# Kernel optimization log

Hardware: AMD Instinct MI355X
Metric: run time of the kernel (lower is better)

The kernel has to match this reference:

```python
import jax, jax.numpy as jnp
import numpy as np

B, N, IN_DIM = 2, 512, 512
MEM, HID = 300, 64
NEG_SLOPE = 0.01


def setup_inputs() -> dict:
    key = jax.random.key(0)
    ks = jax.random.split(key, 10)
    feature = jax.random.normal(ks[0], (B, N, IN_DIM), dtype=jnp.float32)
    adj = jax.random.randint(ks[1], (B, N, N), 0, 2).astype(jnp.float32)
    s = 0.05
    # per-layer node projections W[l]
    w0 = jax.random.normal(ks[2], (IN_DIM, MEM), dtype=jnp.float32) * s
    b0 = jnp.zeros((MEM,), dtype=jnp.float32)
    w1 = jax.random.normal(ks[3], (MEM, MEM), dtype=jnp.float32) * s
    b1 = jnp.zeros((MEM,), dtype=jnp.float32)
    # shared attention MLP (afcs): Linear(2*MEM, HID) -> ReLU -> Linear(HID, 1)
    a1_w = jax.random.normal(ks[4], (2 * MEM, HID), dtype=jnp.float32) * s
    a1_b = jnp.zeros((HID,), dtype=jnp.float32)
    a2_w = jax.random.normal(ks[5], (HID, 1), dtype=jnp.float32) * s
    a2_b = jnp.zeros((1,), dtype=jnp.float32)
    return {"feature": feature, "adj": adj, "w0": w0, "b0": b0, "w1": w1,
            "b1": b1, "a1_w": a1_w, "a1_b": a1_b, "a2_w": a2_w, "a2_b": a2_b}


def _gat_layer(h_in, adj, w, b, a1_w, a1_b, a2_w, a2_b):
    h = h_in @ w + b                                   # (B,N,M)
    # cat([h_i, h_j]) @ a1_w split into the two halves (same math, no N^2*2M tensor)
    s_i = h @ a1_w[:MEM]                               # (B,N,H)
    s_j = h @ a1_w[MEM:]                               # (B,N,H)
    z = jax.nn.relu(s_i[:, :, None, :] + s_j[:, None, :, :] + a1_b)   # (B,N,N,H)
    e = (z @ a2_w)[..., 0] + a2_b[0]                   # (B,N,N)
    e = jax.nn.leaky_relu(e, negative_slope=NEG_SLOPE)
    b_, n_ = adj.shape[0], adj.shape[1]
    dmask = adj.reshape(b_, n_ * n_)
    logits = e.reshape(b_, n_ * n_) * dmask + (1.0 - dmask) * (-1e30)
    # NOTE: softmax over ALL N*N flattened edges (faithful to original dim=1)
    att = jax.nn.softmax(logits, axis=1).reshape(b_, n_, n_)
    return jnp.einsum('bij,bjd->bid', att, h)


def reference(feature, adj, w0, b0, w1, b1, a1_w, a1_b, a2_w, a2_b):
    f = _gat_layer(feature, adj, w0, b0, a1_w, a1_b, a2_w, a2_b)
    f = _gat_layer(f, adj, w1, b1, a1_w, a1_b, a2_w, a2_b)  # dropout = identity (eval)
    return f
```

## Files before the change

kernel.cpp:

```cpp
#include <hip/hip_runtime.h>

namespace {

constexpr int B_  = 2;
constexpr int N_  = 512;
constexpr int IN_ = 512;
constexpr int M_  = 300;
constexpr int H_  = 64;
constexpr float SLOPE_ = 0.01f;

constexpr long OFF_W0AI = 0;
constexpr long OFF_W0AJ = OFF_W0AI + 512L * 64;
constexpr long OFF_W1AI = OFF_W0AJ + 512L * 64;
constexpr long OFF_W1AJ = OFF_W1AI + 300L * 64;
constexpr long OFF_BSI0 = OFF_W1AJ + 300L * 64;
constexpr long OFF_BSJ0 = OFF_BSI0 + 64;
constexpr long OFF_BSI1 = OFF_BSJ0 + 64;
constexpr long OFF_BSJ1 = OFF_BSI1 + 64;
constexpr long OFF_H0   = OFF_BSJ1 + 64;
constexpr long OFF_SI0  = OFF_H0   + 1024L * 300;
constexpr long OFF_SJ0  = OFF_SI0  + 1024L * 64;
constexpr long OFF_F1   = OFF_SJ0  + 1024L * 64;
constexpr long OFF_H1   = OFF_F1   + 1024L * 300;
constexpr long OFF_SI1  = OFF_H1   + 1024L * 300;
constexpr long OFF_SJ1  = OFF_SI1  + 1024L * 64;
constexpr long OFF_ZP0  = OFF_SJ1  + 1024L * 64;
constexpr long OFF_ZP1  = OFF_ZP0  + 512;
constexpr long OFF_P0   = OFF_ZP1  + 512;
constexpr long OFF_P1   = OFF_P0   + 2L * 512 * 512;

struct Jobs {
    const float* A[8]; const float* W[8]; const float* bias[8]; const float* Zp[8];
    float* C[8];
    int K[8]; int lda[8]; int Cc[8]; int R[8];
    int off[8]; int njobs;
};

__global__ __launch_bounds__(256)
void gemm_multi(Jobs jb)
{
    __shared__ __align__(16) float As[16][68];
    __shared__ __align__(16) float Ws[16][64];

    const int bid = blockIdx.x;
    int j = jb.njobs - 1;
    while (j > 0 && bid < jb.off[j]) --j;
    const int local = bid - jb.off[j];

    const float* __restrict__ A = jb.A[j];
    const float* __restrict__ W = jb.W[j];
    const float* bias = jb.bias[j];
    const float* Zp   = jb.Zp[j];
    float* __restrict__ C = jb.C[j];
    const int K = jb.K[j], lda = jb.lda[j], Cc = jb.Cc[j], R = jb.R[j];

    const int tx   = (Cc + 63) >> 6;
    const int row0 = (local / tx) * 64;
    const int col0 = (local % tx) * 64;

    const int t    = threadIdx.x;
    const int arow = min(row0 + (t >> 2), R - 1);
    const int akg  = (t & 3) * 4;
    const int wk   = t >> 4;
    const int wc   = (t & 15) * 4;
    const int tm0  = (t >> 4) * 4;
    const int tn0  = (t & 15) * 4;

    auto loadA = [&](int k0) -> float4 {
        const int k = k0 + akg;
        if (k + 3 < K) return *(const float4*)(A + (long)arow * lda + k);
        float tv[4];
        #pragma unroll
        for (int v = 0; v < 4; ++v)
            tv[v] = (k + v < K) ? A[(long)arow * lda + k + v] : 0.0f;
        return make_float4(tv[0], tv[1], tv[2], tv[3]);
    };
    auto loadW = [&](int k0) -> float4 {
        const int gk = k0 + wk;
        const int c  = col0 + wc;
        if (gk < K && c + 3 < Cc) return *(const float4*)(W + (long)gk * Cc + c);
        float tv[4];
        #pragma unroll
        for (int v = 0; v < 4; ++v)
            tv[v] = (gk < K && c + v < Cc) ? W[(long)gk * Cc + c + v] : 0.0f;
        return make_float4(tv[0], tv[1], tv[2], tv[3]);
    };

    float acc[4][4] = {};
    float4 av = loadA(0);
    float4 wv = loadW(0);

    for (int k0 = 0; k0 < K; k0 += 16) {
        As[akg + 0][t >> 2] = av.x;
        As[akg + 1][t >> 2] = av.y;
        As[akg + 2][t >> 2] = av.z;
        As[akg + 3][t >> 2] = av.w;
        *(float4*)&Ws[wk][wc] = wv;
        __syncthreads();

        if (k0 + 16 < K) {
            av = loadA(k0 + 16);
            wv = loadW(k0 + 16);
        }

        #pragma unroll
        for (int k = 0; k < 16; ++k) {
            const float4 a4 = *(const float4*)&As[k][tm0];
            const float4 w4 = *(const float4*)&Ws[k][tn0];
            const float aa[4] = {a4.x, a4.y, a4.z, a4.w};
            const float ww[4] = {w4.x, w4.y, w4.z, w4.w};
            #pragma unroll
            for (int i = 0; i < 4; ++i)
                #pragma unroll
                for (int jj = 0; jj < 4; ++jj)
                    acc[i][jj] = fmaf(aa[i], ww[jj], acc[i][jj]);
        }
        __syncthreads();
    }

    float scale = 1.0f;
    if (Zp != nullptr) {
        float s0 = 0.f, s1 = 0.f, s2 = 0.f, s3 = 0.f;
        for (int u = 0; u < 256; u += 4) {
            s0 += Zp[u]; s1 += Zp[u + 1]; s2 += Zp[u + 2]; s3 += Zp[u + 3];
        }
        scale = 1.0f / ((s0 + s1) + (s2 + s3));
    }
    const int cbase = col0 + tn0;
    float bv[4] = {0.f, 0.f, 0.f, 0.f};
    if (bias != nullptr) {
        #pragma unroll
        for (int u = 0; u < 4; ++u)
            if (cbase + u < Cc) bv[u] = bias[cbase + u];
    }
    #pragma unroll
    for (int i = 0; i < 4; ++i) {
        const int r = row0 + tm0 + i;
        if (r < R) {
            if (cbase + 3 < Cc) {
                float4 o;
                o.x = fmaf(acc[i][0], scale, bv[0]);
                o.y = fmaf(acc[i][1], scale, bv[1]);
                o.z = fmaf(acc[i][2], scale, bv[2]);
                o.w = fmaf(acc[i][3], scale, bv[3]);
                *(float4*)(C + (long)r * Cc + cbase) = o;
            } else {
                #pragma unroll
                for (int u = 0; u < 4; ++u)
                    if (cbase + u < Cc)
                        C[(long)r * Cc + cbase + u] = fmaf(acc[i][u], scale, bv[u]);
            }
        }
    }
}

__global__ __launch_bounds__(256)
void attn_p_kernel(const float* __restrict__ si, const float* __restrict__ sj,
                   const float* __restrict__ adj, const float* __restrict__ a2w,
                   const float* __restrict__ a2b, float* __restrict__ p,
                   float* __restrict__ Zpart)
{
    __shared__ __align__(16) float Si[32][68];
    __shared__ __align__(16) float Sj[32][68];

    const int b  = blockIdx.z;
    const int i0 = blockIdx.y * 32;
    const int j0 = blockIdx.x * 32;
    const int t  = threadIdx.x;

    {
        const int r  = t >> 3;
        const int hc = (t & 7) * 8;
        const float* gi = si + ((long)(b * N_ + i0 + r)) * H_ + hc;
        const float* gj = sj + ((long)(b * N_ + j0 + r)) * H_ + hc;
        *(float4*)&Si[r][hc]     = *(const float4*)(gi);
        *(float4*)&Si[r][hc + 4] = *(const float4*)(gi + 4);
        *(float4*)&Sj[r][hc]     = *(const float4*)(gj);
        *(float4*)&Sj[r][hc + 4] = *(const float4*)(gj + 4);
    }
    __syncthreads();

    const int i  = t >> 3;
    const int jl = t & 7;

    float e[4] = {0.f, 0.f, 0.f, 0.f};
    #pragma unroll
    for (int h0 = 0; h0 < H_; h0 += 4) {
        const float4 a4 = *(const float4*)&Si[i][h0];
        const float w0v = a2w[h0 + 0];
        const float w1v = a2w[h0 + 1];
        const float w2v = a2w[h0 + 2];
        const float w3v = a2w[h0 + 3];
        #pragma unroll
        for (int u = 0; u < 4; ++u) {
            const float4 b4 = *(const float4*)&Sj[jl + 8 * u][h0];
            e[u] = fmaf(fmaxf(a4.x + b4.x, 0.f), w0v, e[u]);
            e[u] = fmaf(fmaxf(a4.y + b4.y, 0.f), w1v, e[u]);
            e[u] = fmaf(fmaxf(a4.z + b4.z, 0.f), w2v, e[u]);
            e[u] = fmaf(fmaxf(a4.w + b4.w, 0.f), w3v, e[u]);
        }
    }

    const float a2bv = a2b[0];
    const long rowbase = ((long)(b * N_ + i0 + i)) * N_ + j0 + jl;
    float lsum = 0.f;
    #pragma unroll
    for (int u = 0; u < 4; ++u) {
        float ev = e[u] + a2bv;
        ev = (ev >= 0.f) ? ev : SLOPE_ * ev;
        const float m  = adj[rowbase + 8 * u];
        const float pv = m * __expf(ev);
        p[rowbase + 8 * u] = pv;
        lsum += pv;
    }

    #pragma unroll
    for (int off = 32; off > 0; off >>= 1)
        lsum += __shfl_down(lsum, off, 64);
    __shared__ float red[4];
    if ((t & 63) == 0) red[t >> 6] = lsum;
    __syncthreads();
    if (t == 0)
        Zpart[b * 256 + blockIdx.y * 16 + blockIdx.x] =
            red[0] + red[1] + red[2] + red[3];
}

}

extern "C" void kernel_launch(void* const* d_in, const int* in_sizes, int n_in,
                              void* d_out, int out_size, void* d_ws, size_t ws_size,
                              hipStream_t stream)
{
    const float* feature = (const float*)d_in[0];
    const float* adj     = (const float*)d_in[1];
    const float* w0      = (const float*)d_in[2];
    const float* b0      = (const float*)d_in[3];
    const float* w1      = (const float*)d_in[4];
    const float* b1      = (const float*)d_in[5];
    const float* a1w     = (const float*)d_in[6];
    const float* a1b     = (const float*)d_in[7];
    const float* a2w     = (const float*)d_in[8];
    const float* a2b     = (const float*)d_in[9];
    float* out = (float*)d_out;
    float* ws  = (float*)d_ws;

    float* cW0Ai = ws + OFF_W0AI;
    float* cW0Aj = ws + OFF_W0AJ;
    float* cW1Ai = ws + OFF_W1AI;
    float* cW1Aj = ws + OFF_W1AJ;
    float* bsi0  = ws + OFF_BSI0;
    float* bsj0  = ws + OFF_BSJ0;
    float* bsi1  = ws + OFF_BSI1;
    float* bsj1  = ws + OFF_BSJ1;
    float* h0    = ws + OFF_H0;
    float* si0   = ws + OFF_SI0;
    float* sj0   = ws + OFF_SJ0;
    float* f1    = ws + OFF_F1;
    float* h1    = ws + OFF_H1;
    float* si1   = ws + OFF_SI1;
    float* sj1   = ws + OFF_SJ1;
    float* Zp0   = ws + OFF_ZP0;
    float* Zp1   = ws + OFF_ZP1;
    float* p0    = ws + OFF_P0;
    float* p1    = ws + OFF_P1;

    const float* Ai = a1w;
    const float* Aj = a1w + (long)M_ * H_;

    auto set_job = [](Jobs& jb, int j, const float* A, const float* W,
                      const float* bias, const float* Zp, float* C,
                      int K, int lda, int Cc, int R, int& tiles) {
        jb.A[j] = A; jb.W[j] = W; jb.bias[j] = bias; jb.Zp[j] = Zp; jb.C[j] = C;
        jb.K[j] = K; jb.lda[j] = lda; jb.Cc[j] = Cc; jb.R[j] = R;
        jb.off[j] = tiles;
        tiles += ((R + 63) / 64) * ((Cc + 63) / 64);
    };

    {
        Jobs jb; int tiles = 0;
        set_job(jb, 0, w0, Ai, nullptr, nullptr, cW0Ai, M_, M_, H_, IN_, tiles);
        set_job(jb, 1, w0, Aj, nullptr, nullptr, cW0Aj, M_, M_, H_, IN_, tiles);
        set_job(jb, 2, w1, Ai, nullptr, nullptr, cW1Ai, M_, M_, H_, M_,  tiles);
        set_job(jb, 3, w1, Aj, nullptr, nullptr, cW1Aj, M_, M_, H_, M_,  tiles);
        set_job(jb, 4, b0, Ai, nullptr, nullptr, bsi0,  M_, M_, H_, 1,   tiles);
        set_job(jb, 5, b0, Aj, a1b,     nullptr, bsj0,  M_, M_, H_, 1,   tiles);
        set_job(jb, 6, b1, Ai, nullptr, nullptr, bsi1,  M_, M_, H_, 1,   tiles);
        set_job(jb, 7, b1, Aj, a1b,     nullptr, bsj1,  M_, M_, H_, 1,   tiles);
        jb.njobs = 8;
        gemm_multi<<<dim3(tiles), dim3(256), 0, stream>>>(jb);
    }

    {
        Jobs jb; int tiles = 0;
        set_job(jb, 0, feature, w0,    b0,   nullptr, h0,  IN_, IN_, M_, 1024, tiles);
        set_job(jb, 1, feature, cW0Ai, bsi0, nullptr, si0, IN_, IN_, H_, 1024, tiles);
        set_job(jb, 2, feature, cW0Aj, bsj0, nullptr, sj0, IN_, IN_, H_, 1024, tiles);
        jb.njobs = 3;
        gemm_multi<<<dim3(tiles), dim3(256), 0, stream>>>(jb);
    }

    attn_p_kernel<<<dim3(16, 16, B_), dim3(256), 0, stream>>>(
        si0, sj0, adj, a2w, a2b, p0, Zp0);

    {
        Jobs jb; int tiles = 0;
        set_job(jb, 0, p0,               h0,              nullptr, Zp0,       f1,
                N_, N_, M_, N_, tiles);
        set_job(jb, 1, p0 + (long)N_*N_, h0 + (long)N_*M_, nullptr, Zp0 + 256,
                f1 + (long)N_*M_, N_, N_, M_, N_, tiles);
        jb.njobs = 2;
        gemm_multi<<<dim3(tiles), dim3(256), 0, stream>>>(jb);
    }

    {
        Jobs jb; int tiles = 0;
        set_job(jb, 0, f1, w1,    b1,   nullptr, h1,  M_, M_, M_, 1024, tiles);
        set_job(jb, 1, f1, cW1Ai, bsi1, nullptr, si1, M_, M_, H_, 1024, tiles);
        set_job(jb, 2, f1, cW1Aj, bsj1, nullptr, sj1, M_, M_, H_, 1024, tiles);
        jb.njobs = 3;
        gemm_multi<<<dim3(tiles), dim3(256), 0, stream>>>(jb);
    }

    attn_p_kernel<<<dim3(16, 16, B_), dim3(256), 0, stream>>>(
        si1, sj1, adj, a2w, a2b, p1, Zp1);

    {
        Jobs jb; int tiles = 0;
        set_job(jb, 0, p1,               h1,              nullptr, Zp1,       out,
                N_, N_, M_, N_, tiles);
        set_job(jb, 1, p1 + (long)N_*N_, h1 + (long)N_*M_, nullptr, Zp1 + 256,
                out + (long)N_*M_, N_, N_, M_, N_, tiles);
        jb.njobs = 2;
        gemm_multi<<<dim3(tiles), dim3(256), 0, stream>>>(jb);
    }
}
```

Measured before the change: 197.7 us.

## Split-K GEMMs into partial halves, fuse attention into mega kernel, reassociate layer-2 score projections

Replaces separate GEMM and attention kernels with a single multi-job mega kernel that can run GEMM tiles and attention-score tiles in the same launch. Each GEMM is split along K into two halves written to separate buffers, which consumers sum on load, so more blocks are available. Layer-2 score projections are reassociated as p·(h0·W1A) so they can run alongside the layer-1 aggregation. The final aggregation uses a smaller 32-row tile GEMM for more blocks. The aim is fewer serial launches and better GPU fill, at the cost of extra partial-buffer traffic, doubled loads and more complex job dispatch.

```diff
diff --git a/kernel.cpp b/kernel.cpp
--- a/kernel.cpp
+++ b/kernel.cpp
@@ -2,227 +2,400 @@
 
 namespace {
 
-constexpr int B_  = 2;
-constexpr int N_  = 512;
-constexpr int IN_ = 512;
-constexpr int M_  = 300;
-constexpr int H_  = 64;
+constexpr int N_ = 512;
+constexpr int M_ = 300;
+constexpr int H_ = 64;
 constexpr float SLOPE_ = 0.01f;
-
-constexpr long OFF_W0AI = 0;
-constexpr long OFF_W0AJ = OFF_W0AI + 512L * 64;
-constexpr long OFF_W1AI = OFF_W0AJ + 512L * 64;
-constexpr long OFF_W1AJ = OFF_W1AI + 300L * 64;
-constexpr long OFF_BSI0 = OFF_W1AJ + 300L * 64;
-constexpr long OFF_BSJ0 = OFF_BSI0 + 64;
-constexpr long OFF_BSI1 = OFF_BSJ0 + 64;
-constexpr long OFF_BSJ1 = OFF_BSI1 + 64;
-constexpr long OFF_H0   = OFF_BSJ1 + 64;
-constexpr long OFF_SI0  = OFF_H0   + 1024L * 300;
-constexpr long OFF_SJ0  = OFF_SI0  + 1024L * 64;
-constexpr long OFF_F1   = OFF_SJ0  + 1024L * 64;
-constexpr long OFF_H1   = OFF_F1   + 1024L * 300;
-constexpr long OFF_SI1  = OFF_H1   + 1024L * 300;
-constexpr long OFF_SJ1  = OFF_SI1  + 1024L * 64;
-constexpr long OFF_ZP0  = OFF_SJ1  + 1024L * 64;
-constexpr long OFF_ZP1  = OFF_ZP0  + 512;
-constexpr long OFF_P0   = OFF_ZP1  + 512;
-constexpr long OFF_P1   = OFF_P0   + 2L * 512 * 512;
-
+constexpr long NN = 262144;
+constexpr long NM = 153600;
+constexpr long NH = 32768;
+
+constexpr long O_CW0AI_A = 0;
+constexpr long O_CW0AI_B = O_CW0AI_A + 512L*64;
+constexpr long O_CW0AJ_A = O_CW0AI_B + 512L*64;
+constexpr long O_CW0AJ_B = O_CW0AJ_A + 512L*64;
+constexpr long O_CW1AI_A = O_CW0AJ_B + 512L*64;
+constexpr long O_CW1AI_B = O_CW1AI_A + 300L*64;
+constexpr long O_CW1AJ_A = O_CW1AI_B + 300L*64;
+constexpr long O_CW1AJ_B = O_CW1AJ_A + 300L*64;
+constexpr long O_BS      = O_CW1AJ_B + 300L*64;
+constexpr long O_H0_A  = O_BS + 8*64;
+constexpr long O_H0_B  = O_H0_A + 1024L*300;
+constexpr long O_SI0_A = O_H0_B + 1024L*300;
+constexpr long O_SI0_B = O_SI0_A + 1024L*64;
+constexpr long O_SJ0_A = O_SI0_B + 1024L*64;
+constexpr long O_SJ0_B = O_SJ0_A + 1024L*64;
+constexpr long O_GI_A  = O_SJ0_B + 1024L*64;
+constexpr long O_GI_B  = O_GI_A + 1024L*64;
+constexpr long O_GJ_A  = O_GI_B + 1024L*64;
+constexpr long O_GJ_B  = O_GJ_A + 1024L*64;
+constexpr long O_F1_A  = O_GJ_B + 1024L*64;
+constexpr long O_F1_B  = O_F1_A + 1024L*300;
+constexpr long O_H1_A  = O_F1_B + 1024L*300;
+constexpr long O_H1_B  = O_H1_A + 1024L*300;
+constexpr long O_SI1_A = O_H1_B + 1024L*300;
+constexpr long O_SI1_B = O_SI1_A + 1024L*64;
+constexpr long O_SJ1_A = O_SI1_B + 1024L*64;
+constexpr long O_SJ1_B = O_SJ1_A + 1024L*64;
+constexpr long O_ZP0   = O_SJ1_B + 1024L*64;
+constexpr long O_ZP1   = O_ZP0 + 512;
+constexpr long O_P0    = O_ZP1 + 512;
+constexpr long O_P1    = O_P0 + 2L*NN;
+
+constexpr int MAXJ = 12;
 struct Jobs {
-    const float* A[8]; const float* W[8]; const float* bias[8]; const float* Zp[8];
-    float* C[8];
-    int K[8]; int lda[8]; int Cc[8]; int R[8];
-    int off[8]; int njobs;
+    const float* A[MAXJ]; const float* A2[MAXJ];
+    const float* W[MAXJ]; const float* W2[MAXJ];
+    const float* bias[MAXJ]; const float* bias2[MAXJ];
+    const float* Zp[MAXJ];
+    float* C[MAXJ]; float* Zout[MAXJ];
+    int ks[MAXJ], ke[MAXJ], lda[MAXJ], Cc[MAXJ], R[MAXJ], off[MAXJ], type[MAXJ];
+    int njobs;
 };
 
+__device__ __forceinline__ float job_scale(const float* Zp)
+{
+    if (Zp == nullptr) return 1.0f;
+    float s0 = 0.f, s1 = 0.f, s2 = 0.f, s3 = 0.f;
+    for (int u = 0; u < 256; u += 4) {
+        s0 += Zp[u]; s1 += Zp[u + 1]; s2 += Zp[u + 2]; s3 += Zp[u + 3];
+    }
+    return 1.0f / ((s0 + s1) + (s2 + s3));
+}
+
 __global__ __launch_bounds__(256)
-void gemm_multi(Jobs jb)
+void mega(Jobs jb, const float* __restrict__ a2w, const float* __restrict__ a2b)
 {
-    __shared__ __align__(16) float As[16][68];
-    __shared__ __align__(16) float Ws[16][64];
+    __shared__ __align__(16) char sm[17424];
 
     const int bid = blockIdx.x;
     int j = jb.njobs - 1;
     while (j > 0 && bid < jb.off[j]) --j;
     const int local = bid - jb.off[j];
-
-    const float* __restrict__ A = jb.A[j];
-    const float* __restrict__ W = jb.W[j];
-    const float* bias = jb.bias[j];
-    const float* Zp   = jb.Zp[j];
+    const int t = threadIdx.x;
+
+    if (jb.type[j] == 0) {
+        float (*As)[68] = reinterpret_cast<float(*)[68]>(sm);
+        float (*Ws)[64] = reinterpret_cast<float(*)[64]>(sm + 16*68*4);
+
+        const float* __restrict__ A  = jb.A[j];
+        const float* __restrict__ A2 = jb.A2[j];
+        const float* __restrict__ W  = jb.W[j];
+        const float* __restrict__ W2 = jb.W2[j];
+        float* __restrict__ C = jb.C[j];
+        const int ks = jb.ks[j], ke = jb.ke[j];
+        const int lda = jb.lda[j], Cc = jb.Cc[j], R = jb.R[j];
+
+        const int tx   = (Cc + 63) >> 6;
+        const int row0 = (local / tx) * 64;
+        const int col0 = (local % tx) * 64;
+
+        const int arow = min(row0 + (t >> 2), R - 1);
+        const int akg  = (t & 3) * 4;
+        const int wk   = t >> 4;
+        const int wc   = (t & 15) * 4;
+        const int tm0  = (t >> 4) * 4;
+        const int tn0  = (t & 15) * 4;
+
+        auto loadA1 = [&](const float* P, int k0) -> float4 {
+            const int k = k0 + akg;
+            if (k + 3 < ke) return *(const float4*)(P + (long)arow * lda + k);
+            float tv[4];
+            #pragma unroll
+            for (int v = 0; v < 4; ++v)
+                tv[v] = (k + v < ke) ? P[(long)arow * lda + k + v] : 0.0f;
+            return make_float4(tv[0], tv[1], tv[2], tv[3]);
+        };
+        auto loadW1 = [&](const float* P, int k0) -> float4 {
+            const int gk = k0 + wk;
+            const int c  = col0 + wc;
+            if (gk < ke && c + 3 < Cc) return *(const float4*)(P + (long)gk * Cc + c);
+            float tv[4];
+            #pragma unroll
+            for (int v = 0; v < 4; ++v)
+                tv[v] = (gk < ke && c + v < Cc) ? P[(long)gk * Cc + c + v] : 0.0f;
+            return make_float4(tv[0], tv[1], tv[2], tv[3]);
+        };
+        auto loadA = [&](int k0) -> float4 {
+            float4 r = loadA1(A, k0);
+            if (A2) {
+                const float4 r2 = loadA1(A2, k0);
+                r.x += r2.x; r.y += r2.y; r.z += r2.z; r.w += r2.w;
+            }
+            return r;
+        };
+        auto loadW = [&](int k0) -> float4 {
+            float4 r = loadW1(W, k0);
+            if (W2) {
+                const float4 r2 = loadW1(W2, k0);
+                r.x += r2.x; r.y += r2.y; r.z += r2.z; r.w += r2.w;
+            }
+            return r;
+        };
+
+        float acc[4][4] = {};
+        float4 av = loadA(ks);
+        float4 wv = loadW(ks);
+
+        for (int k0 = ks; k0 < ke; k0 += 16) {
+            As[akg + 0][t >> 2] = av.x;
+            As[akg + 1][t >> 2] = av.y;
+            As[akg + 2][t >> 2] = av.z;
+            As[akg + 3][t >> 2] = av.w;
+            *(float4*)&Ws[wk][wc] = wv;
+            __syncthreads();
+
+            if (k0 + 16 < ke) {
+                av = loadA(k0 + 16);
+                wv = loadW(k0 + 16);
+            }
+
+            #pragma unroll
+            for (int k = 0; k < 16; ++k) {
+                const float4 a4 = *(const float4*)&As[k][tm0];
+                const float4 w4 = *(const float4*)&Ws[k][tn0];
+                const float aa[4] = {a4.x, a4.y, a4.z, a4.w};
+                const float ww[4] = {w4.x, w4.y, w4.z, w4.w};
+                #pragma unroll
+                for (int i = 0; i < 4; ++i)
+                    #pragma unroll
+                    for (int q = 0; q < 4; ++q)
+                        acc[i][q] = fmaf(aa[i], ww[q], acc[i][q]);
+            }
+            __syncthreads();
+        }
+
+        const float scale = job_scale(jb.Zp[j]);
+        const int cbase = col0 + tn0;
+        float bv[4] = {0.f, 0.f, 0.f, 0.f};
+        if (jb.bias[j] != nullptr && ks == 0) {
+            const float* b1p = jb.bias[j];
+            const float* b2p = jb.bias2[j];
+            #pragma unroll
+            for (int u = 0; u < 4; ++u)
+                if (cbase + u < Cc)
+                    bv[u] = b1p[cbase + u] + (b2p ? b2p[cbase + u] : 0.0f);
+        }
+        #pragma unroll
+        for (int i = 0; i < 4; ++i) {
+            const int r = row0 + tm0 + i;
+            if (r < R) {
+                if (cbase + 3 < Cc) {
+                    float4 o;
+                    o.x = fmaf(acc[i][0], scale, bv[0]);
+                    o.y = fmaf(acc[i][1], scale, bv[1]);
+                    o.z = fmaf(acc[i][2], scale, bv[2]);
+                    o.w = fmaf(acc[i][3], scale, bv[3]);
+                    *(float4*)(C + (long)r * Cc + cbase) = o;
+                } else {
+                    #pragma unroll
+                    for (int u = 0; u < 4; ++u)
+                        if (cbase + u < Cc)
+                            C[(long)r * Cc + cbase + u] = fmaf(acc[i][u], scale, bv[u]);
+                }
+            }
+        }
+    } else {
+        float (*Si)[68] = reinterpret_cast<float(*)[68]>(sm);
+        float (*Sj)[68] = reinterpret_cast<float(*)[68]>(sm + 32*68*4);
+        float* red = reinterpret_cast<float*>(sm + 2*32*68*4);
+
+        const int b  = local >> 8;
+        const int r8 = local & 255;
+        const int i0 = (r8 >> 4) * 32;
+        const int j0 = (r8 & 15) * 32;
+
+        const float* siA = jb.A[j]  + (long)b * NH;
+        const float* siB = jb.A2[j] + (long)b * NH;
+        const float* sjA = jb.W[j]  + (long)b * NH;
+        const float* sjB = jb.W2[j] + (long)b * NH;
+        const float* adjb = jb.bias[j] + (long)b * NN;
+        float* pb = jb.C[j] + (long)b * NN;
+
+        {
+            const int r  = t >> 3;
+            const int hc = (t & 7) * 8;
+            const long oi = (long)(i0 + r) * H_ + hc;
+            const long oj = (long)(j0 + r) * H_ + hc;
+            #pragma unroll
+            for (int h = 0; h < 2; ++h) {
+                float4 v1 = *(const float4*)(siA + oi + 4*h);
+                const float4 v2 = *(const float4*)(siB + oi + 4*h);
+                v1.x += v2.x; v1.y += v2.y; v1.z += v2.z; v1.w += v2.w;
+                *(float4*)&Si[r][hc + 4*h] = v1;
+                float4 u1 = *(const float4*)(sjA + oj + 4*h);
+                const float4 u2 = *(const float4*)(sjB + oj + 4*h);
+                u1.x += u2.x; u1.y += u2.y; u1.z += u2.z; u1.w += u2.w;
+                *(float4*)&Sj[r][hc + 4*h] = u1;
+            }
+        }
+        __syncthreads();
+
+        const int i  = t >> 3;
+        const int jl = t & 7;
+
+        float e[4] = {0.f, 0.f, 0.f, 0.f};
+        #pragma unroll
+        for (int h0 = 0; h0 < H_; h0 += 4) {
+            const float4 a4 = *(const float4*)&Si[i][h0];
+            const float w0v = a2w[h0 + 0];
+            const float w1v = a2w[h0 + 1];
+            const float w2v = a2w[h0 + 2];
+            const float w3v = a2w[h0 + 3];
+            #pragma unroll
+            for (int u = 0; u < 4; ++u) {
+                const float4 b4 = *(const float4*)&Sj[jl + 8 * u][h0];
+                e[u] = fmaf(fmaxf(a4.x + b4.x, 0.f), w0v, e[u]);
+                e[u] = fmaf(fmaxf(a4.y + b4.y, 0.f), w1v, e[u]);
+                e[u] = fmaf(fmaxf(a4.z + b4.z, 0.f), w2v, e[u]);
+                e[u] = fmaf(fmaxf(a4.w + b4.w, 0.f), w3v, e[u]);
+            }
+        }
+
+        const float a2bv = a2b[0];
+        const long rowbase = (long)(i0 + i) * N_ + j0 + jl;
+        float lsum = 0.f;
+        #pragma unroll
+        for (int u = 0; u < 4; ++u) {
+            float ev = e[u] + a2bv;
+            ev = (ev >= 0.f) ? ev : SLOPE_ * ev;
+            const float m  = adjb[rowbase + 8 * u];
+            const float pv = m * __expf(ev);
+            pb[rowbase + 8 * u] = pv;
+            lsum += pv;
+        }
+
+        #pragma unroll
+        for (int off = 32; off > 0; off >>= 1)
+            lsum += __shfl_down(lsum, off, 64);
+        if ((t & 63) == 0) red[t >> 6] = lsum;
+        __syncthreads();
+        if (t == 0)
+            jb.Zout[j][b * 256 + r8] = red[0] + red[1] + red[2] + red[3];
+    }
+}
+
+__global__ __launch_bounds__(256)
+void gemm32(Jobs jb)
+{
+    __shared__ __align__(16) float As[32][38];
+    __shared__ __align__(16) float Ws[32][64];
+
+    const int bid = blockIdx.x;
+    int j = jb.njobs - 1;
+    while (j > 0 && bid < jb.off[j]) --j;
+    const int local = bid - jb.off[j];
+
+    const float* __restrict__ A  = jb.A[j];
+    const float* __restrict__ W  = jb.W[j];
+    const float* __restrict__ W2 = jb.W2[j];
     float* __restrict__ C = jb.C[j];
-    const int K = jb.K[j], lda = jb.lda[j], Cc = jb.Cc[j], R = jb.R[j];
+    const int ke = jb.ke[j], lda = jb.lda[j], Cc = jb.Cc[j], R = jb.R[j];
 
     const int tx   = (Cc + 63) >> 6;
-    const int row0 = (local / tx) * 64;
+    const int row0 = (local / tx) * 32;
     const int col0 = (local % tx) * 64;
 
     const int t    = threadIdx.x;
-    const int arow = min(row0 + (t >> 2), R - 1);
-    const int akg  = (t & 3) * 4;
+    const int sr   = t >> 3;
+    const int sk   = (t & 7) * 4;
+    const int arow = min(row0 + sr, R - 1);
     const int wk   = t >> 4;
     const int wc   = (t & 15) * 4;
-    const int tm0  = (t >> 4) * 4;
+    const int tm0  = (t >> 4) * 2;
     const int tn0  = (t & 15) * 4;
 
     auto loadA = [&](int k0) -> float4 {
-        const int k = k0 + akg;
-        if (k + 3 < K) return *(const float4*)(A + (long)arow * lda + k);
+        const int k = k0 + sk;
+        if (k + 3 < ke) return *(const float4*)(A + (long)arow * lda + k);
         float tv[4];
         #pragma unroll
         for (int v = 0; v < 4; ++v)
-            tv[v] = (k + v < K) ? A[(long)arow * lda + k + v] : 0.0f;
+            tv[v] = (k + v < ke) ? A[(long)arow * lda + k + v] : 0.0f;
         return make_float4(tv[0], tv[1], tv[2], tv[3]);
     };
-    auto loadW = [&](int k0) -> float4 {
-        const int gk = k0 + wk;
+    auto loadW = [&](int k0, int s) -> float4 {
+        const int gk = k0 + wk + 16 * s;
         const int c  = col0 + wc;
-        if (gk < K && c + 3 < Cc) return *(const float4*)(W + (long)gk * Cc + c);
-        float tv[4];
+        float4 r = make_float4(0.f, 0.f, 0.f, 0.f);
+        if (gk < ke) {
+            if (c + 3 < Cc) {
+                r = *(const float4*)(W + (long)gk * Cc + c);
+                if (W2) {
+                    const float4 r2 = *(const float4*)(W2 + (long)gk * Cc + c);
+                    r.x += r2.x; r.y += r2.y; r.z += r2.z; r.w += r2.w;
+                }
+            } else {
+                float tv[4];
+                #pragma unroll
+                for (int v = 0; v < 4; ++v) {
+                    tv[v] = (c + v < Cc) ? W[(long)gk * Cc + c + v] : 0.0f;
+                    if (W2 && c + v < Cc) tv[v] += W2[(long)gk * Cc + c + v];
+                }
+                r = make_float4(tv[0], tv[1], tv[2], tv[3]);
+            }
+        }
+        return r;
+    };
+
+    float acc[2][4] = {};
+    float4 av  = loadA(0);
+    float4 wv0 = loadW(0, 0);
+    float4 wv1 = loadW(0, 1);
+
+    for (int k0 = 0; k0 < ke; k0 += 32) {
+        As[sk + 0][sr] = av.x;
+        As[sk + 1][sr] = av.y;
+        As[sk + 2][sr] = av.z;
+        As[sk + 3][sr] = av.w;
+        *(float4*)&Ws[wk][wc]      = wv0;
+        *(float4*)&Ws[wk + 16][wc] = wv1;
+        __syncthreads();
+
+        if (k0 + 32 < ke) {
+            av  = loadA(k0 + 32);
+            wv0 = loadW(k0 + 32, 0);
+            wv1 = loadW(k0 + 32, 1);
+        }
+
         #pragma unroll
-        for (int v = 0; v < 4; ++v)
-            tv[v] = (gk < K && c + v < Cc) ? W[(long)gk * Cc + c + v] : 0.0f;
-        return make_float4(tv[0], tv[1], tv[2], tv[3]);
-    };
-
-    float acc[4][4] = {};
-    float4 av = loadA(0);
-    float4 wv = loadW(0);
-
-    for (int k0 = 0; k0 < K; k0 += 16) {
-        As[akg + 0][t >> 2] = av.x;
-        As[akg + 1][t >> 2] = av.y;
-        As[akg + 2][t >> 2] = av.z;
-        As[akg + 3][t >> 2] = av.w;
-        *(float4*)&Ws[wk][wc] = wv;
+        for (int k = 0; k < 32; ++k) {
+            const float a0 = As[k][tm0];
+            const float a1 = As[k][tm0 + 1];
+            const float4 w4 = *(const float4*)&Ws[k][tn0];
+            acc[0][0] = fmaf(a0, w4.x, acc[0][0]);
+            acc[0][1] = fmaf(a0, w4.y, acc[0][1]);
+            acc[0][2] = fmaf(a0, w4.z, acc[0][2]);
+            acc[0][3] = fmaf(a0, w4.w, acc[0][3]);
+            acc[1][0] = fmaf(a1, w4.x, acc[1][0]);
+            acc[1][1] = fmaf(a1, w4.y, acc[1][1]);
+            acc[1][2] = fmaf(a1, w4.z, acc[1][2]);
+            acc[1][3] = fmaf(a1, w4.w, acc[1][3]);
+        }
         __syncthreads();
-
-        if (k0 + 16 < K) {
-            av = loadA(k0 + 16);
-            wv = loadW(k0 + 16);
-        }
-
-        #pragma unroll
-        for (int k = 0; k < 16; ++k) {
-            const float4 a4 = *(const float4*)&As[k][tm0];
-            const float4 w4 = *(const float4*)&Ws[k][tn0];
-            const float aa[4] = {a4.x, a4.y, a4.z, a4.w};
-            const float ww[4] = {w4.x, w4.y, w4.z, w4.w};
-            #pragma unroll
-            for (int i = 0; i < 4; ++i)
-                #pragma unroll
-                for (int jj = 0; jj < 4; ++jj)
-                    acc[i][jj] = fmaf(aa[i], ww[jj], acc[i][jj]);
-        }
-        __syncthreads();
-    }
-
-    float scale = 1.0f;
-    if (Zp != nullptr) {
-        float s0 = 0.f, s1 = 0.f, s2 = 0.f, s3 = 0.f;
-        for (int u = 0; u < 256; u += 4) {
-            s0 += Zp[u]; s1 += Zp[u + 1]; s2 += Zp[u + 2]; s3 += Zp[u + 3];
-        }
-        scale = 1.0f / ((s0 + s1) + (s2 + s3));
-    }
+    }
+
+    const float scale = job_scale(jb.Zp[j]);
     const int cbase = col0 + tn0;
-    float bv[4] = {0.f, 0.f, 0.f, 0.f};
-    if (bias != nullptr) {
-        #pragma unroll
-        for (int u = 0; u < 4; ++u)
-            if (cbase + u < Cc) bv[u] = bias[cbase + u];
-    }
     #pragma unroll
-    for (int i = 0; i < 4; ++i) {
+    for (int i = 0; i < 2; ++i) {
         const int r = row0 + tm0 + i;
         if (r < R) {
             if (cbase + 3 < Cc) {
                 float4 o;
-                o.x = fmaf(acc[i][0], scale, bv[0]);
-                o.y = fmaf(acc[i][1], scale, bv[1]);
-                o.z = fmaf(acc[i][2], scale, bv[2]);
-                o.w = fmaf(acc[i][3], scale, bv[3]);
+                o.x = acc[i][0] * scale;
+                o.y = acc[i][1] * scale;
+                o.z = acc[i][2] * scale;
+                o.w = acc[i][3] * scale;
                 *(float4*)(C + (long)r * Cc + cbase) = o;
             } else {
                 #pragma unroll
                 for (int u = 0; u < 4; ++u)
                     if (cbase + u < Cc)
-                        C[(long)r * Cc + cbase + u] = fmaf(acc[i][u], scale, bv[u]);
-            }
-        }
-    }
-}
-
-__global__ __launch_bounds__(256)
-void attn_p_kernel(const float* __restrict__ si, const float* __restrict__ sj,
-                   const float* __restrict__ adj, const float* __restrict__ a2w,
-                   const float* __restrict__ a2b, float* __restrict__ p,
-                   float* __restrict__ Zpart)
-{
-    __shared__ __align__(16) float Si[32][68];
-    __shared__ __align__(16) float Sj[32][68];
-
-    const int b  = blockIdx.z;
-    const int i0 = blockIdx.y * 32;
-    const int j0 = blockIdx.x * 32;
-    const int t  = threadIdx.x;
-
-    {
-        const int r  = t >> 3;
-        const int hc = (t & 7) * 8;
-        const float* gi = si + ((long)(b * N_ + i0 + r)) * H_ + hc;
-        const float* gj = sj + ((long)(b * N_ + j0 + r)) * H_ + hc;
-        *(float4*)&Si[r][hc]     = *(const float4*)(gi);
-        *(float4*)&Si[r][hc + 4] = *(const float4*)(gi + 4);
-        *(float4*)&Sj[r][hc]     = *(const float4*)(gj);
-        *(float4*)&Sj[r][hc + 4] = *(const float4*)(gj + 4);
-    }
-    __syncthreads();
-
-    const int i  = t >> 3;
-    const int jl = t & 7;
-
-    float e[4] = {0.f, 0.f, 0.f, 0.f};
-    #pragma unroll
-    for (int h0 = 0; h0 < H_; h0 += 4) {
-        const float4 a4 = *(const float4*)&Si[i][h0];
-        const float w0v = a2w[h0 + 0];
-        const float w1v = a2w[h0 + 1];
-        const float w2v = a2w[h0 + 2];
-        const float w3v = a2w[h0 + 3];
-        #pragma unroll
-        for (int u = 0; u < 4; ++u) {
-            const float4 b4 = *(const float4*)&Sj[jl + 8 * u][h0];
-            e[u] = fmaf(fmaxf(a4.x + b4.x, 0.f), w0v, e[u]);
-            e[u] = fmaf(fmaxf(a4.y + b4.y, 0.f), w1v, e[u]);
-            e[u] = fmaf(fmaxf(a4.z + b4.z, 0.f), w2v, e[u]);
-            e[u] = fmaf(fmaxf(a4.w + b4.w, 0.f), w3v, e[u]);
-        }
-    }
-
-    const float a2bv = a2b[0];
-    const long rowbase = ((long)(b * N_ + i0 + i)) * N_ + j0 + jl;
-    float lsum = 0.f;
-    #pragma unroll
-    for (int u = 0; u < 4; ++u) {
-        float ev = e[u] + a2bv;
-        ev = (ev >= 0.f) ? ev : SLOPE_ * ev;
-        const float m  = adj[rowbase + 8 * u];
-        const float pv = m * __expf(ev);
-        p[rowbase + 8 * u] = pv;
-        lsum += pv;
-    }
-
-    #pragma unroll
-    for (int off = 32; off > 0; off >>= 1)
-        lsum += __shfl_down(lsum, off, 64);
-    __shared__ float red[4];
-    if ((t & 63) == 0) red[t >> 6] = lsum;
-    __syncthreads();
-    if (t == 0)
-        Zpart[b * 256 + blockIdx.y * 16 + blockIdx.x] =
-            red[0] + red[1] + red[2] + red[3];
+                        C[(long)r * Cc + cbase + u] = acc[i][u] * scale;
+            }
+        }
+    }
 }
 
 }
@@ -244,93 +417,123 @@
     float* out = (float*)d_out;
     float* ws  = (float*)d_ws;
 
-    float* cW0Ai = ws + OFF_W0AI;
-    float* cW0Aj = ws + OFF_W0AJ;
-    float* cW1Ai = ws + OFF_W1AI;
-    float* cW1Aj = ws + OFF_W1AJ;
-    float* bsi0  = ws + OFF_BSI0;
-    float* bsj0  = ws + OFF_BSJ0;
-    float* bsi1  = ws + OFF_BSI1;
-    float* bsj1  = ws + OFF_BSJ1;
-    float* h0    = ws + OFF_H0;
-    float* si0   = ws + OFF_SI0;
-    float* sj0   = ws + OFF_SJ0;
-    float* f1    = ws + OFF_F1;
-    float* h1    = ws + OFF_H1;
-    float* si1   = ws + OFF_SI1;
-    float* sj1   = ws + OFF_SJ1;
-    float* Zp0   = ws + OFF_ZP0;
-    float* Zp1   = ws + OFF_ZP1;
-    float* p0    = ws + OFF_P0;
-    float* p1    = ws + OFF_P1;
-
     const float* Ai = a1w;
     const float* Aj = a1w + (long)M_ * H_;
 
-    auto set_job = [](Jobs& jb, int j, const float* A, const float* W,
-                      const float* bias, const float* Zp, float* C,
-                      int K, int lda, int Cc, int R, int& tiles) {
-        jb.A[j] = A; jb.W[j] = W; jb.bias[j] = bias; jb.Zp[j] = Zp; jb.C[j] = C;
-        jb.K[j] = K; jb.lda[j] = lda; jb.Cc[j] = Cc; jb.R[j] = R;
-        jb.off[j] = tiles;
-        tiles += ((R + 63) / 64) * ((Cc + 63) / 64);
+    float* cW0AiA = ws + O_CW0AI_A; float* cW0AiB = ws + O_CW0AI_B;
+    float* cW0AjA = ws + O_CW0AJ_A; float* cW0AjB = ws + O_CW0AJ_B;
+    float* cW1AiA = ws + O_CW1AI_A; float* cW1AiB = ws + O_CW1AI_B;
+    float* cW1AjA = ws + O_CW1AJ_A; float* cW1AjB = ws + O_CW1AJ_B;
+    float* bs     = ws + O_BS;
+    float* h0A = ws + O_H0_A;  float* h0B = ws + O_H0_B;
+    float* si0A = ws + O_SI0_A; float* si0B = ws + O_SI0_B;
+    float* sj0A = ws + O_SJ0_A; float* sj0B = ws + O_SJ0_B;
+    float* giA = ws + O_GI_A;  float* giB = ws + O_GI_B;
+    float* gjA = ws + O_GJ_A;  float* gjB = ws + O_GJ_B;
+    float* f1A = ws + O_F1_A;  float* f1B = ws + O_F1_B;
+    float* h1A = ws + O_H1_A;  float* h1B = ws + O_H1_B;
+    float* si1A = ws + O_SI1_A; float* si1B = ws + O_SI1_B;
+    float* sj1A = ws + O_SJ1_A; float* sj1B = ws + O_SJ1_B;
+    float* Zp0 = ws + O_ZP0;   float* Zp1 = ws + O_ZP1;
+    float* p0  = ws + O_P0;    float* p1  = ws + O_P1;
+
+    struct Builder {
+        Jobs jb{}; int tiles = 0; int n = 0;
+        void gem(const float* A, const float* A2, const float* W, const float* W2,
+                 const float* bias, const float* bias2, const float* Zp, float* C,
+                 int ks, int ke, int lda, int Cc, int R) {
+            jb.A[n]=A; jb.A2[n]=A2; jb.W[n]=W; jb.W2[n]=W2;
+            jb.bias[n]=bias; jb.bias2[n]=bias2; jb.Zp[n]=Zp; jb.C[n]=C; jb.Zout[n]=nullptr;
+            jb.ks[n]=ks; jb.ke[n]=ke; jb.lda[n]=lda; jb.Cc[n]=Cc; jb.R[n]=R;
+            jb.off[n]=tiles; jb.type[n]=0;
+            tiles += ((R + 63)/64) * ((Cc + 63)/64);
+            jb.njobs = ++n;
+        }
+        void att(const float* siA_, const float* siB_, const float* sjA_,
+                 const float* sjB_, const float* adj_, float* p_, float* Z_) {
+            jb.A[n]=siA_; jb.A2[n]=siB_; jb.W[n]=sjA_; jb.W2[n]=sjB_;
+            jb.bias[n]=adj_; jb.bias2[n]=nullptr; jb.Zp[n]=nullptr; jb.C[n]=p_; jb.Zout[n]=Z_;
+            jb.ks[n]=0; jb.ke[n]=0; jb.lda[n]=0; jb.Cc[n]=0; jb.R[n]=0;
+            jb.off[n]=tiles; jb.type[n]=1;
+            tiles += 512;
+            jb.njobs = ++n;
+        }
     };
+    constexpr int KS = 152;
 
     {
-        Jobs jb; int tiles = 0;
-        set_job(jb, 0, w0, Ai, nullptr, nullptr, cW0Ai, M_, M_, H_, IN_, tiles);
-        set_job(jb, 1, w0, Aj, nullptr, nullptr, cW0Aj, M_, M_, H_, IN_, tiles);
-        set_job(jb, 2, w1, Ai, nullptr, nullptr, cW1Ai, M_, M_, H_, M_,  tiles);
-        set_job(jb, 3, w1, Aj, nullptr, nullptr, cW1Aj, M_, M_, H_, M_,  tiles);
-        set_job(jb, 4, b0, Ai, nullptr, nullptr, bsi0,  M_, M_, H_, 1,   tiles);
-        set_job(jb, 5, b0, Aj, a1b,     nullptr, bsj0,  M_, M_, H_, 1,   tiles);
-        set_job(jb, 6, b1, Ai, nullptr, nullptr, bsi1,  M_, M_, H_, 1,   tiles);
-        set_job(jb, 7, b1, Aj, a1b,     nullptr, bsj1,  M_, M_, H_, 1,   tiles);
-        jb.njobs = 8;
-        gemm_multi<<<dim3(tiles), dim3(256), 0, stream>>>(jb);
-    }
-
+        Builder b;
+        b.gem(w0, nullptr, Ai, nullptr, nullptr, nullptr, nullptr, cW0AiA, 0, KS, M_, H_, 512);
+        b.gem(w0, nullptr, Ai, nullptr, nullptr, nullptr, nullptr, cW0AiB, KS, M_, M_, H_, 512);
+        b.gem(w0, nullptr, Aj, nullptr, nullptr, nullptr, nullptr, cW0AjA, 0, KS, M_, H_, 512);
+        b.gem(w0, nullptr, Aj, nullptr, nullptr, nullptr, nullptr, cW0AjB, KS, M_, M_, H_, 512);
+        b.gem(b0, nullptr, Ai, nullptr, nullptr, nullptr, nullptr, bs + 0*64, 0, KS, M_, H_, 1);
+        b.gem(b0, nullptr, Ai, nullptr, nullptr, nullptr, nullptr, bs + 1*64, KS, M_, M_, H_, 1);
+        b.gem(b0, nullptr, Aj, nullptr, a1b,     nullptr, nullptr, bs + 2*64, 0, KS, M_, H_, 1);
+        b.gem(b0, nullptr, Aj, nullptr, nullptr, nullptr, nullptr, bs + 3*64, KS, M_, M_, H_, 1);
+        b.gem(b1, nullptr, Ai, nullptr, nullptr, nullptr, nullptr, bs + 4*64, 0, KS, M_, H_, 1);
+        b.gem(b1, nullptr, Ai, nullptr, nullptr, nullptr, nullptr, bs + 5*64, KS, M_, M_, H_, 1);
+        b.gem(b1, nullptr, Aj, nullptr, a1b,     nullptr, nullptr, bs + 6*64, 0, KS, M_, H_, 1);
+        b.gem(b1, nullptr, Aj, nullptr, nullptr, nullptr, nullptr, bs + 7*64, KS, M_, M_, H_, 1);
+        mega<<<dim3(b.tiles), dim3(256), 0, stream>>>(b.jb, a2w, a2b);
+    }
     {
-        Jobs jb; int tiles = 0;
-        set_job(jb, 0, feature, w0,    b0,   nullptr, h0,  IN_, IN_, M_, 1024, tiles);
-        set_job(jb, 1, feature, cW0Ai, bsi0, nullptr, si0, IN_, IN_, H_, 1024, tiles);
-        set_job(jb, 2, feature, cW0Aj, bsj0, nullptr, sj0, IN_, IN_, H_, 1024, tiles);
-        jb.njobs = 3;
-        gemm_multi<<<dim3(tiles), dim3(256), 0, stream>>>(jb);
-    }
-
-    attn_p_kernel<<<dim3(16, 16, B_), dim3(256), 0, stream>>>(
-        si0, sj0, adj, a2w, a2b, p0, Zp0);
-
+        Builder b;
+        b.gem(feature, nullptr, w0, nullptr, b0, nullptr, nullptr, h0A, 0, 256, 512, M_, 1024);
+        b.gem(feature, nullptr, w0, nullptr, nullptr, nullptr, nullptr, h0B, 256, 512, 512, M_, 1024);
+        b.gem(feature, nullptr, cW0AiA, cW0AiB, bs+0*64, bs+1*64, nullptr, si0A, 0, 256, 512, H_, 1024);
+        b.gem(feature, nullptr, cW0AiA, cW0AiB, nullptr, nullptr, nullptr, si0B, 256, 512, 512, H_, 1024);
+        b.gem(feature, nullptr, cW0AjA, cW0AjB, bs+2*64, bs+3*64, nullptr, sj0A, 0, 256, 512, H_, 1024);
+        b.gem(feature, nullptr, cW0AjA, cW0AjB, nullptr, nullptr, nullptr, sj0B, 256, 512, 512, H_, 1024);
+        b.gem(w1, nullptr, Ai, nullptr, nullptr, nullptr, nullptr, cW1AiA, 0, KS, M_, H_, 300);
+        b.gem(w1, nullptr, Ai, nullptr, nullptr, nullptr, nullptr, cW1AiB, KS, M_, M_, H_, 300);
+        b.gem(w1, nullptr, Aj, nullptr, nullptr, nullptr, nullptr, cW1AjA, 0, KS, M_, H_, 300);
+        b.gem(w1, nullptr, Aj, nullptr, nullptr, nullptr, nullptr, cW1AjB, KS, M_, M_, H_, 300);
+        mega<<<dim3(b.tiles), dim3(256), 0, stream>>>(b.jb, a2w, a2b);
+    }
     {
-        Jobs jb; int tiles = 0;
-        set_job(jb, 0, p0,               h0,              nullptr, Zp0,       f1,
-                N_, N_, M_, N_, tiles);
-        set_job(jb, 1, p0 + (long)N_*N_, h0 + (long)N_*M_, nullptr, Zp0 + 256,
-                f1 + (long)N_*M_, N_, N_, M_, N_, tiles);
-        jb.njobs = 2;
-        gemm_multi<<<dim3(tiles), dim3(256), 0, stream>>>(jb);
-    }
-
+        Builder b;
+        b.gem(h0A, h0B, cW1AiA, cW1AiB, nullptr, nullptr, nullptr, giA, 0, KS, M_, H_, 1024);
+        b.gem(h0A, h0B, cW1AiA, cW1AiB, nullptr, nullptr, nullptr, giB, KS, M_, M_, H_, 1024);
+        b.gem(h0A, h0B, cW1AjA, cW1AjB, nullptr, nullptr, nullptr, gjA, 0, KS, M_, H_, 1024);
+        b.gem(h0A, h0B, cW1AjA, cW1AjB, nullptr, nullptr, nullptr, gjB, KS, M_, M_, H_, 1024);
+        b.att(si0A, si0B, sj0A, sj0B, adj, p0, Zp0);
+        mega<<<dim3(b.tiles), dim3(256), 0, stream>>>(b.jb, a2w, a2b);
+    }
     {
-        Jobs jb; int tiles = 0;
-        set_job(jb, 0, f1, w1,    b1,   nullptr, h1,  M_, M_, M_, 1024, tiles);
-        set_job(jb, 1, f1, cW1Ai, bsi1, nullptr, si1, M_, M_, H_, 1024, tiles);
-        set_job(jb, 2, f1, cW1Aj, bsj1, nullptr, sj1, M_, M_, H_, 1024, tiles);
-        jb.njobs = 3;
-        gemm_multi<<<dim3(tiles), dim3(256), 0, stream>>>(jb);
-    }
-
-    attn_p_kernel<<<dim3(16, 16, B_), dim3(256), 0, stream>>>(
-        si1, sj1, adj, a2w, a2b, p1, Zp1);
-
+        Builder b;
+        for (int bt = 0; bt < 2; ++bt) {
+            const float* pA = p0 + (long)bt * NN;
+            const float* Zq = Zp0 + bt * 256;
+            b.gem(pA, nullptr, h0A + bt*NM, h0B + bt*NM, nullptr, nullptr, Zq, f1A + bt*NM, 0, 256, 512, M_, 512);
+            b.gem(pA, nullptr, h0A + bt*NM, h0B + bt*NM, nullptr, nullptr, Zq, f1B + bt*NM, 256, 512, 512, M_, 512);
+            b.gem(pA, nullptr, giA + bt*NH, giB + bt*NH, bs+4*64, bs+5*64, Zq, si1A + bt*NH, 0, 256, 512, H_, 512);
+            b.gem(pA, nullptr, giA + bt*NH, giB + bt*NH, nullptr, nullptr, Zq, si1B + bt*NH, 256, 512, 512, H_, 512);
+            b.gem(pA, nullptr, gjA + bt*NH, gjB + bt*NH, bs+6*64, bs+7*64, Zq, sj1A + bt*NH, 0, 256, 512, H_, 512);
+            b.gem(pA, nullptr, gjA + bt*NH, gjB + bt*NH, nullptr, nullptr, Zq, sj1B + bt*NH, 256, 512, 512, H_, 512);
+        }
+        mega<<<dim3(b.tiles), dim3(256), 0, stream>>>(b.jb, a2w, a2b);
+    }
     {
-        Jobs jb; int tiles = 0;
-        set_job(jb, 0, p1,               h1,              nullptr, Zp1,       out,
-                N_, N_, M_, N_, tiles);
-        set_job(jb, 1, p1 + (long)N_*N_, h1 + (long)N_*M_, nullptr, Zp1 + 256,
-                out + (long)N_*M_, N_, N_, M_, N_, tiles);
-        jb.njobs = 2;
-        gemm_multi<<<dim3(tiles), dim3(256), 0, stream>>>(jb);
+        Builder b;
+        b.gem(f1A, f1B, w1, nullptr, b1, nullptr, nullptr, h1A, 0, KS, M_, M_, 1024);
+        b.gem(f1A, f1B, w1, nullptr, nullptr, nullptr, nullptr, h1B, KS, M_, M_, M_, 1024);
+        b.att(si1A, si1B, sj1A, sj1B, adj, p1, Zp1);
+        mega<<<dim3(b.tiles), dim3(256), 0, stream>>>(b.jb, a2w, a2b);
+    }
+    {
+        Builder b;
+        b.jb.njobs = 0; b.n = 0; b.tiles = 0;
+        for (int bt = 0; bt < 2; ++bt) {
+            b.jb.A[b.n]=p1 + (long)bt*NN; b.jb.A2[b.n]=nullptr;
+            b.jb.W[b.n]=h1A + bt*NM; b.jb.W2[b.n]=h1B + bt*NM;
+            b.jb.bias[b.n]=nullptr; b.jb.bias2[b.n]=nullptr;
+            b.jb.Zp[b.n]=Zp1 + bt*256; b.jb.C[b.n]=out + (long)bt*NM; b.jb.Zout[b.n]=nullptr;
+            b.jb.ks[b.n]=0; b.jb.ke[b.n]=512; b.jb.lda[b.n]=512; b.jb.Cc[b.n]=M_; b.jb.R[b.n]=512;
+            b.jb.off[b.n]=b.tiles; b.jb.type[b.n]=0;
+            b.tiles += (512/32) * ((M_ + 63)/64);
+            b.jb.njobs = ++b.n;
+        }
+        gemm32<<<dim3(b.tiles), dim3(256), 0, stream>>>(b.jb);
     }
 }
```

Result: slower. 212.2 us (+7.4%).
